# Kernel optimization log

Measured on AMD Instinct MI355X. Metric: run time of the kernel, lower is better.

Reference implementation:

```python
import jax, jax.numpy as jnp
import numpy as np

N_NODES = 100000
N_EDGES = 1600000
N_GRAPHS = 5000
NODE_DIM = 16
EDGE_DIM = 16
HID = 20


def setup_inputs() -> dict:
    key = jax.random.key(0)
    ks = jax.random.split(key, 12)
    edge_index = jax.random.randint(ks[0], (2, N_EDGES), 0, N_NODES)
    node_attr = jax.random.normal(ks[1], (N_NODES, NODE_DIM), dtype=jnp.float32)
    edge_attr = jax.random.normal(ks[2], (N_EDGES, EDGE_DIM), dtype=jnp.float32)
    batch = jnp.sort(jax.random.randint(ks[3], (N_NODES,), 0, N_GRAPHS))
    s = 0.1
    W_msg = jax.random.normal(ks[4], (2 * NODE_DIM + EDGE_DIM, HID), dtype=jnp.float32) * s
    b_msg = jnp.zeros((HID,), dtype=jnp.float32)
    W1 = jax.random.normal(ks[5], (HID, 10), dtype=jnp.float32) * s
    b1 = jnp.zeros((10,), dtype=jnp.float32)
    W2 = jax.random.normal(ks[6], (10, 10), dtype=jnp.float32) * s
    b2 = jnp.zeros((10,), dtype=jnp.float32)
    W3 = jax.random.normal(ks[7], (10, 1), dtype=jnp.float32) * s
    b3 = jnp.zeros((1,), dtype=jnp.float32)
    return {"edge_index": edge_index, "node_attr": node_attr, "edge_attr": edge_attr,
            "batch": batch, "W_msg": W_msg, "b_msg": b_msg, "W1": W1, "b1": b1,
            "W2": W2, "b2": b2, "W3": W3, "b3": b3}


def reference(edge_index, node_attr, edge_attr, batch,
              W_msg, b_msg, W1, b1, W2, b2, W3, b3):
    src, dst = edge_index[0], edge_index[1]
    # MPL_1: gather -> linear -> relu -> scatter-sum to destination nodes
    feats = jnp.concatenate([node_attr[src], node_attr[dst], edge_attr], axis=-1)  # [E, 48]
    msg = jax.nn.relu(feats @ W_msg + b_msg)  # [E, 20]
    x = jax.ops.segment_sum(msg, dst, num_segments=N_NODES)  # [N, 20]
    # node MLP + graph pooling (segment_coo sum over batch) + graph MLP
    x = jax.nn.relu(x @ W1 + b1)  # [N, 10]
    g = jax.ops.segment_sum(x, batch, num_segments=N_GRAPHS)  # [G, 10]
    g = jax.nn.relu(g @ W2 + b2)
    return g @ W3 + b3  # [G, 1]
```

## Files before the change

### kernel.cpp

```cpp
#include <hip/hip_runtime.h>

constexpr int NN = 100000;
constexpr int NE = 1600000;
constexpr int NG = 5000;
constexpr int BKT = 64;
constexpr int NBKT = (NN + BKT - 1) / BKT;
constexpr int NB = 128;
constexpr int CHUNK = NE / NB;

typedef float v2f __attribute__((ext_vector_type(2)));

constexpr size_t OFF_G  = 0;
constexpr size_t OFF_BH = 50048;
constexpr size_t OFF_ST = OFF_BH + (size_t)NB * NBKT;
constexpr size_t OFF_PM = OFF_ST + NBKT + 1;

__global__ __launch_bounds__(256) void k_hist(const int* __restrict__ ei,
                                              int* __restrict__ bh,
                                              float* __restrict__ g) {
  __shared__ int lh[NBKT];
  for (int i = threadIdx.x; i < NBKT; i += 256) lh[i] = 0;
  __syncthreads();
  const int* dstp = ei + NE;
  int s = blockIdx.x * CHUNK;
  for (int i = s + threadIdx.x; i < s + CHUNK; i += 256)
    atomicAdd(&lh[dstp[i] >> 6], 1);
  int gid = blockIdx.x * 256 + threadIdx.x;
  if (gid < 12500) ((float4*)g)[gid] = make_float4(0.f, 0.f, 0.f, 0.f);
  __syncthreads();
  int* out = bh + (size_t)blockIdx.x * NBKT;
  for (int k = threadIdx.x; k < NBKT; k += 256) out[k] = lh[k];
}

__global__ __launch_bounds__(256) void k_btot(const int* __restrict__ bh,
                                              int* __restrict__ starts) {
  int k = blockIdx.x * 256 + threadIdx.x;
  if (k >= NBKT) return;
  int tot = 0;
  for (int b = 0; b < NB; b += 4) {
    int a0 = bh[(size_t)(b    ) * NBKT + k];
    int a1 = bh[(size_t)(b + 1) * NBKT + k];
    int a2 = bh[(size_t)(b + 2) * NBKT + k];
    int a3 = bh[(size_t)(b + 3) * NBKT + k];
    tot += a0 + a1 + a2 + a3;
  }
  starts[k] = tot;
}

__global__ __launch_bounds__(1024) void k_sscan(int* __restrict__ starts) {
  __shared__ int s0[1024], s1[1024];
  int t = threadIdx.x;
  int k0 = 2 * t, k1 = 2 * t + 1;
  int tot0 = (k0 < NBKT) ? starts[k0] : 0;
  int tot1 = (k1 < NBKT) ? starts[k1] : 0;
  int ssum = tot0 + tot1;
  int* cur = s0; int* nxt = s1;
  cur[t] = ssum;
  __syncthreads();
  for (int off = 1; off < 1024; off <<= 1) {
    int v = cur[t];
    if (t >= off) v += cur[t - off];
    nxt[t] = v;
    __syncthreads();
    int* tmp = cur; cur = nxt; nxt = tmp;
  }
  int excl = cur[t] - ssum;
  if (k0 < NBKT) starts[k0] = excl;
  if (k1 <= NBKT) starts[k1] = excl + tot0;
}

__global__ __launch_bounds__(256) void k_bases(int* __restrict__ bh,
                                               const int* __restrict__ starts) {
  int k = blockIdx.x * 256 + threadIdx.x;
  if (k >= NBKT) return;
  int run = starts[k];
  for (int b = 0; b < NB; ++b) {
    size_t idx = (size_t)b * NBKT + k;
    int v = bh[idx];
    bh[idx] = run;
    run += v;
  }
}

__global__ __launch_bounds__(256) void k_scatter(const int* __restrict__ ei,
                                                 const int* __restrict__ bh,
                                                 int* __restrict__ perm) {
  __shared__ int base[NBKT];
  __shared__ int cnt[NBKT];
  const int* row = bh + (size_t)blockIdx.x * NBKT;
  for (int k = threadIdx.x; k < NBKT; k += 256) { base[k] = row[k]; cnt[k] = 0; }
  __syncthreads();
  const int* dstp = ei + NE;
  int s = blockIdx.x * CHUNK;
  for (int i = s + threadIdx.x; i < s + CHUNK; i += 256) {
    int d = dstp[i];
    int k = d >> 6;
    int r = atomicAdd(&cnt[k], 1);
    perm[base[k] + r] = i | ((d & 63) << 24);
  }
}

#define PK4(V, K0) \
  a0 = __builtin_elementwise_fma(v2f{(V).x, (V).x}, W[K0+0], a0); \
  a1 = __builtin_elementwise_fma(v2f{(V).y, (V).y}, W[K0+1], a1); \
  a2 = __builtin_elementwise_fma(v2f{(V).z, (V).z}, W[K0+2], a2); \
  a3 = __builtin_elementwise_fma(v2f{(V).w, (V).w}, W[K0+3], a3);

__global__ __launch_bounds__(256, 2) void k_edge(
    const int* __restrict__ ei,
    const float* __restrict__ nattr,
    const float* __restrict__ eattr,
    const float* __restrict__ Wm,
    const float* __restrict__ bm,
    const int* __restrict__ batch,
    const float* __restrict__ W1,
    const float* __restrict__ b1,
    const int* __restrict__ perm,
    const int* __restrict__ starts,
    float* __restrict__ g) {
  __shared__ float xt[20 * 65];
  __shared__ float gb[64 * 10];
  __shared__ int s_se[2];
  __shared__ int s_bmin;
  for (int i = threadIdx.x; i < 20 * 65; i += 256) xt[i] = 0.f;
  for (int i = threadIdx.x; i < 640; i += 256) gb[i] = 0.f;
  if (threadIdx.x < 2) s_se[threadIdx.x] = starts[blockIdx.x + threadIdx.x];
  int nbase = blockIdx.x * BKT;
  if (threadIdx.x == 0) s_bmin = batch[nbase];
  __syncthreads();
  int is = s_se[0], ie = s_se[1];

  int wave = threadIdx.x >> 6;
  int lane = threadIdx.x & 63;
  int ep = lane / 10;
  int jp = lane - ep * 10;
  bool act = ep < 6;
  int epc = act ? ep : 0;

  v2f W[48];
#pragma unroll
  for (int k = 0; k < 48; ++k)
    W[k] = v2f{Wm[k * 20 + 2 * jp], Wm[k * 20 + 2 * jp + 1]};
#pragma unroll
  for (int k = 0; k < 48; ++k) asm volatile("" : "+v"(W[k]));
  v2f bj = {bm[2 * jp], bm[2 * jp + 1]};

  int base = is + wave * 6;
  int iC = base + epc;
  int pC = 0, sC = 0;
  float4 e0, e1, e2, e3, n0, n1, n2, n3;
  if (base < ie) {
    pC = perm[min(iC, ie - 1)];
    sC = ei[pC & 0xFFFFFF];
    const float4* pe = (const float4*)(eattr + (size_t)(pC & 0xFFFFFF) * 16);
    const float4* ps = (const float4*)(nattr + (size_t)sC * 16);
    e0 = pe[0]; e1 = pe[1]; e2 = pe[2]; e3 = pe[3];
    n0 = ps[0]; n1 = ps[1]; n2 = ps[2]; n3 = ps[3];
  }
  while (base < ie) {
    int baseN = base + 24;
    int iN = baseN + epc;
    int pN = 0, sN = 0;
    if (baseN < ie) {
      pN = perm[min(iN, ie - 1)];
      sN = ei[pN & 0xFFFFFF];
    }
    const float4* peN = (const float4*)(eattr + (size_t)(pN & 0xFFFFFF) * 16);
    const float4* psN = (const float4*)(nattr + (size_t)sN * 16);
    float4 e0N = peN[0], e1N = peN[1], e2N = peN[2], e3N = peN[3];
    float4 n0N = psN[0], n1N = psN[1], n2N = psN[2], n3N = psN[3];

    int dl = (pC >> 24) & 63;
    const float4* pd = (const float4*)(nattr + (size_t)(nbase + dl) * 16);
    float4 u0 = pd[0], u1 = pd[1], u2 = pd[2], u3 = pd[3];

    v2f a0 = {0.f, 0.f}, a1 = {0.f, 0.f}, a2 = {0.f, 0.f}, a3 = {0.f, 0.f};
    PK4(n0, 0)  PK4(n1, 4)  PK4(n2, 8)  PK4(n3, 12)
    PK4(u0, 16) PK4(u1, 20) PK4(u2, 24) PK4(u3, 28)
    PK4(e0, 32) PK4(e1, 36) PK4(e2, 40) PK4(e3, 44)
    v2f r = ((a0 + a1) + (a2 + a3)) + bj;

    bool valid = act && (iC < ie);
    float m0 = fmaxf(r.x, 0.f);
    float m1 = fmaxf(r.y, 0.f);
    if (valid && m0 > 0.f) atomicAdd(&xt[(2 * jp) * 65 + dl], m0);
    if (valid && m1 > 0.f) atomicAdd(&xt[(2 * jp + 1) * 65 + dl], m1);

    base = baseN; iC = iN; pC = pN; sC = sN;
    e0 = e0N; e1 = e1N; e2 = e2N; e3 = e3N;
    n0 = n0N; n1 = n1N; n2 = n2N; n3 = n3N;
  }
  __syncthreads();

  int nn = min(BKT, NN - nbase);
  int bmin = s_bmin;
  if (threadIdx.x < 64 && (int)threadIdx.x < nn) {
    int node = threadIdx.x;
    float xi[20];
#pragma unroll
    for (int j = 0; j < 20; ++j) xi[j] = xt[j * 65 + node];
    float acc[10];
#pragma unroll
    for (int j = 0; j < 10; ++j) acc[j] = b1[j];
#pragma unroll
    for (int k = 0; k < 20; ++k) {
      float fk = xi[k];
#pragma unroll
      for (int j = 0; j < 10; ++j) acc[j] = fmaf(fk, W1[k * 10 + j], acc[j]);
    }
    int bn = batch[nbase + node];
    int d = bn - bmin;
    if (d < 64) {
#pragma unroll
      for (int j = 0; j < 10; ++j) {
        float m = fmaxf(acc[j], 0.f);
        if (m > 0.f) atomicAdd(&gb[d * 10 + j], m);
      }
    } else {
#pragma unroll
      for (int j = 0; j < 10; ++j) {
        float m = fmaxf(acc[j], 0.f);
        if (m > 0.f) unsafeAtomicAdd(&g[(size_t)bn * 10 + j], m);
      }
    }
  }
  __syncthreads();
  int glim = min(640, NG * 10 - bmin * 10);
  float* gp = g + (size_t)bmin * 10;
  for (int idx = threadIdx.x; idx < glim; idx += 256) {
    float v = gb[idx];
    if (v != 0.f) unsafeAtomicAdd(&gp[idx], v);
  }
}

__global__ __launch_bounds__(256) void k_graph(
    const float* __restrict__ g,
    const float* __restrict__ W2, const float* __restrict__ b2,
    const float* __restrict__ W3, const float* __restrict__ b3,
    float* __restrict__ out) {
  int i = blockIdx.x * 256 + threadIdx.x;
  if (i >= NG) return;
  float gi[10];
  const float2* pg = (const float2*)(g + (size_t)i * 10);
#pragma unroll
  for (int k = 0; k < 5; ++k) { float2 v = pg[k]; gi[2*k] = v.x; gi[2*k+1] = v.y; }
  float o = b3[0];
#pragma unroll
  for (int j = 0; j < 10; ++j) {
    float a = b2[j];
#pragma unroll
    for (int k = 0; k < 10; ++k) a = fmaf(gi[k], W2[k * 10 + j], a);
    o = fmaf(fmaxf(a, 0.f), W3[j], o);
  }
  out[i] = o;
}

extern "C" void kernel_launch(void* const* d_in, const int* in_sizes, int n_in,
                              void* d_out, int out_size, void* d_ws, size_t ws_size,
                              hipStream_t stream) {
  const int*   ei    = (const int*)  d_in[0];
  const float* nattr = (const float*)d_in[1];
  const float* eattr = (const float*)d_in[2];
  const int*   batch = (const int*)  d_in[3];
  const float* Wm    = (const float*)d_in[4];
  const float* bm    = (const float*)d_in[5];
  const float* W1    = (const float*)d_in[6];
  const float* b1    = (const float*)d_in[7];
  const float* W2    = (const float*)d_in[8];
  const float* b2    = (const float*)d_in[9];
  const float* W3    = (const float*)d_in[10];
  const float* b3    = (const float*)d_in[11];

  float* g      = (float*)d_ws + OFF_G;
  int*   bh     = (int*)d_ws + OFF_BH;
  int*   starts = (int*)d_ws + OFF_ST;
  int*   perm   = (int*)d_ws + OFF_PM;

  constexpr int SCAN_BLKS = (NBKT + 255) / 256;

  k_hist   <<<NB, 256, 0, stream>>>(ei, bh, g);
  k_btot   <<<SCAN_BLKS, 256, 0, stream>>>(bh, starts);
  k_sscan  <<<1, 1024, 0, stream>>>(starts);
  k_bases  <<<SCAN_BLKS, 256, 0, stream>>>(bh, starts);
  k_scatter<<<NB, 256, 0, stream>>>(ei, bh, perm);
  k_edge   <<<NBKT, 256, 0, stream>>>(ei, nattr, eattr, Wm, bm, batch, W1, b1,
                                      perm, starts, g);
  k_graph  <<<(NG + 255) / 256, 256, 0, stream>>>(g, W2, b2, W3, b3, (float*)d_out);
}
```

Before: 438.5 us.

## Move edge-MLP weights to shared memory and raise occupancy in edge kernel

```diff
diff --git a/kernel.cpp b/kernel.cpp
--- a/kernel.cpp
+++ b/kernel.cpp
@@ -100,13 +100,15 @@
   }
 }
 
-#define PK4(V, K0) \
-  a0 = __builtin_elementwise_fma(v2f{(V).x, (V).x}, W[K0+0], a0); \
-  a1 = __builtin_elementwise_fma(v2f{(V).y, (V).y}, W[K0+1], a1); \
-  a2 = __builtin_elementwise_fma(v2f{(V).z, (V).z}, W[K0+2], a2); \
-  a3 = __builtin_elementwise_fma(v2f{(V).w, (V).w}, W[K0+3], a3);
-
-__global__ __launch_bounds__(256, 2) void k_edge(
+#define PK4(V, T) { \
+  float4 wA = wt4[wrow + (T)];     \
+  float4 wB = wt4[wrow + (T) + 1]; \
+  a0 = __builtin_elementwise_fma(v2f{(V).x, (V).x}, v2f{wA.x, wA.y}, a0); \
+  a1 = __builtin_elementwise_fma(v2f{(V).y, (V).y}, v2f{wA.z, wA.w}, a1); \
+  a2 = __builtin_elementwise_fma(v2f{(V).z, (V).z}, v2f{wB.x, wB.y}, a2); \
+  a3 = __builtin_elementwise_fma(v2f{(V).w, (V).w}, v2f{wB.z, wB.w}, a3); }
+
+__global__ __launch_bounds__(256, 5) void k_edge(
     const int* __restrict__ ei,
     const float* __restrict__ nattr,
     const float* __restrict__ eattr,
@@ -120,10 +122,16 @@
     float* __restrict__ g) {
   __shared__ float xt[20 * 65];
   __shared__ float gb[64 * 10];
+  __shared__ float4 wt4[250];
   __shared__ int s_se[2];
   __shared__ int s_bmin;
   for (int i = threadIdx.x; i < 20 * 65; i += 256) xt[i] = 0.f;
   for (int i = threadIdx.x; i < 640; i += 256) gb[i] = 0.f;
+  for (int i = threadIdx.x; i < 240; i += 256) {
+    int j = i / 24, t = i - j * 24, k = 2 * t;
+    wt4[j * 25 + t] = make_float4(Wm[k * 20 + 2 * j],       Wm[k * 20 + 2 * j + 1],
+                                  Wm[(k + 1) * 20 + 2 * j], Wm[(k + 1) * 20 + 2 * j + 1]);
+  }
   if (threadIdx.x < 2) s_se[threadIdx.x] = starts[blockIdx.x + threadIdx.x];
   int nbase = blockIdx.x * BKT;
   if (threadIdx.x == 0) s_bmin = batch[nbase];
@@ -137,58 +145,45 @@
   bool act = ep < 6;
   int epc = act ? ep : 0;
 
-  v2f W[48];
-#pragma unroll
-  for (int k = 0; k < 48; ++k)
-    W[k] = v2f{Wm[k * 20 + 2 * jp], Wm[k * 20 + 2 * jp + 1]};
-#pragma unroll
-  for (int k = 0; k < 48; ++k) asm volatile("" : "+v"(W[k]));
   v2f bj = {bm[2 * jp], bm[2 * jp + 1]};
 
   int base = is + wave * 6;
-  int iC = base + epc;
-  int pC = 0, sC = 0;
-  float4 e0, e1, e2, e3, n0, n1, n2, n3;
+  int p0 = 0, p1 = 0, s0 = 0;
   if (base < ie) {
-    pC = perm[min(iC, ie - 1)];
-    sC = ei[pC & 0xFFFFFF];
-    const float4* pe = (const float4*)(eattr + (size_t)(pC & 0xFFFFFF) * 16);
-    const float4* ps = (const float4*)(nattr + (size_t)sC * 16);
-    e0 = pe[0]; e1 = pe[1]; e2 = pe[2]; e3 = pe[3];
-    n0 = ps[0]; n1 = ps[1]; n2 = ps[2]; n3 = ps[3];
+    p0 = perm[min(base + epc, ie - 1)];
+    s0 = ei[p0 & 0xFFFFFF];
+    int bn = base + 24;
+    p1 = (bn < ie) ? perm[min(bn + epc, ie - 1)] : p0;
   }
   while (base < ie) {
-    int baseN = base + 24;
-    int iN = baseN + epc;
-    int pN = 0, sN = 0;
-    if (baseN < ie) {
-      pN = perm[min(iN, ie - 1)];
-      sN = ei[pN & 0xFFFFFF];
-    }
-    const float4* peN = (const float4*)(eattr + (size_t)(pN & 0xFFFFFF) * 16);
-    const float4* psN = (const float4*)(nattr + (size_t)sN * 16);
-    float4 e0N = peN[0], e1N = peN[1], e2N = peN[2], e3N = peN[3];
-    float4 n0N = psN[0], n1N = psN[1], n2N = psN[2], n3N = psN[3];
-
-    int dl = (pC >> 24) & 63;
+    int b2 = base + 48;
+    int p2 = (b2 < ie) ? perm[min(b2 + epc, ie - 1)] : p1;
+    int sN = (base + 24 < ie) ? ei[p1 & 0xFFFFFF] : s0;
+
+    const float4* pe = (const float4*)(eattr + (size_t)(p0 & 0xFFFFFF) * 16);
+    const float4* ps = (const float4*)(nattr + (size_t)s0 * 16);
+    float4 e0 = pe[0], e1 = pe[1], e2 = pe[2], e3 = pe[3];
+    float4 n0 = ps[0], n1 = ps[1], n2 = ps[2], n3 = ps[3];
+    int dl = (p0 >> 24) & 63;
     const float4* pd = (const float4*)(nattr + (size_t)(nbase + dl) * 16);
     float4 u0 = pd[0], u1 = pd[1], u2 = pd[2], u3 = pd[3];
 
+    int wrow = jp * 25;
+    asm volatile("" : "+v"(wrow));
+
     v2f a0 = {0.f, 0.f}, a1 = {0.f, 0.f}, a2 = {0.f, 0.f}, a3 = {0.f, 0.f};
-    PK4(n0, 0)  PK4(n1, 4)  PK4(n2, 8)  PK4(n3, 12)
-    PK4(u0, 16) PK4(u1, 20) PK4(u2, 24) PK4(u3, 28)
-    PK4(e0, 32) PK4(e1, 36) PK4(e2, 40) PK4(e3, 44)
+    PK4(n0, 0)  PK4(n1, 2)  PK4(n2, 4)  PK4(n3, 6)
+    PK4(u0, 8)  PK4(u1, 10) PK4(u2, 12) PK4(u3, 14)
+    PK4(e0, 16) PK4(e1, 18) PK4(e2, 20) PK4(e3, 22)
     v2f r = ((a0 + a1) + (a2 + a3)) + bj;
 
-    bool valid = act && (iC < ie);
+    bool valid = act && (base + epc < ie);
     float m0 = fmaxf(r.x, 0.f);
     float m1 = fmaxf(r.y, 0.f);
     if (valid && m0 > 0.f) atomicAdd(&xt[(2 * jp) * 65 + dl], m0);
     if (valid && m1 > 0.f) atomicAdd(&xt[(2 * jp + 1) * 65 + dl], m1);
 
-    base = baseN; iC = iN; pC = pN; sC = sN;
-    e0 = e0N; e1 = e1N; e2 = e2N; e3 = e3N;
-    n0 = n0N; n1 = n1N; n2 = n2N; n3 = n3N;
+    base += 24; p0 = p1; p1 = p2; s0 = sN;
   }
   __syncthreads();
 
```

Measured after the change: 380.6 us. 13.2% less time.
